# Kernel tuning notes

Measured on AMD Instinct MI355X. Metric: run time of the kernel, lower is better.

Reference implementation:

```python
import jax, jax.numpy as jnp
import numpy as np

B, A, D, H = 256, 16, 768, 512
LN_EPS = 1e-5


def setup_inputs() -> dict:
    key = jax.random.key(0)
    ks = jax.random.split(key, 8)
    aspects = jax.random.normal(ks[0], (B, A, D), dtype=jnp.float32)
    aspect_mask = jnp.ones((B, A), dtype=bool)
    # relation_gate: Linear(2D->H), ReLU, Dropout(eval=id), Linear(H->1)
    # xavier_uniform with gain=0.1, bias=-2.0 (per the module's custom init)
    lim1 = 0.1 * np.sqrt(6.0 / (2 * D + H))
    lim2 = 0.1 * np.sqrt(6.0 / (H + 1))
    W_g1 = jax.random.uniform(ks[1], (2 * D, H), jnp.float32, -lim1, lim1)
    b_g1 = jnp.full((H,), -2.0, dtype=jnp.float32)
    w_g2 = jax.random.uniform(ks[2], (H,), jnp.float32, -lim2, lim2)
    b_g2 = jnp.asarray(-2.0, dtype=jnp.float32)
    # composition: Linear(2D->H), ReLU, Dropout(eval=id), Linear(H->D), default init scale
    sc1 = 1.0 / np.sqrt(2 * D)
    sc2 = 1.0 / np.sqrt(H)
    W_c1 = jax.random.uniform(ks[3], (2 * D, H), jnp.float32, -sc1, sc1)
    b_c1 = jax.random.uniform(ks[4], (H,), jnp.float32, -sc1, sc1)
    W_c2 = jax.random.uniform(ks[5], (H, D), jnp.float32, -sc2, sc2)
    b_c2 = jax.random.uniform(ks[6], (D,), jnp.float32, -sc2, sc2)
    ln_gamma = jnp.ones((D,), dtype=jnp.float32)
    ln_beta = jnp.zeros((D,), dtype=jnp.float32)
    return {
        "aspects": aspects, "aspect_mask": aspect_mask,
        "W_g1": W_g1, "b_g1": b_g1, "w_g2": w_g2, "b_g2": b_g2,
        "W_c1": W_c1, "b_c1": b_c1, "W_c2": W_c2, "b_c2": b_c2,
        "ln_gamma": ln_gamma, "ln_beta": ln_beta,
    }


def reference(aspects, aspect_mask, W_g1, b_g1, w_g2, b_g2,
              W_c1, b_c1, W_c2, b_c2, ln_gamma, ln_beta):
    b, a, d = aspects.shape
    # cat([x_i, x_j]) @ W == x_i @ W[:D] + x_j @ W[D:]  -> batch all (i,j) pairs at once
    Wg_i, Wg_j = W_g1[:d], W_g1[d:]
    gi = jnp.einsum('bad,dh->bah', aspects, Wg_i)   # [B,A,H]
    gj = jnp.einsum('bad,dh->bah', aspects, Wg_j)   # [B,A,H]
    hg = jax.nn.relu(gi[:, :, None, :] + gj[:, None, :, :] + b_g1)  # [B,A,A,H]
    gate = jax.nn.sigmoid(jnp.einsum('bijh,h->bij', hg, w_g2) + b_g2)  # [B,A,A]
    eye = jnp.eye(a, dtype=bool)
    gate = jnp.where(eye[None], 0.0, gate)  # i==j pair skipped; all_gates diag stays 0

    Wc_i, Wc_j = W_c1[:d], W_c1[d:]
    ci = jnp.einsum('bad,dh->bah', aspects, Wc_i)
    cj = jnp.einsum('bad,dh->bah', aspects, Wc_j)
    hc = jax.nn.relu(ci[:, :, None, :] + cj[:, None, :, :] + b_c1)  # [B,A,A,H]
    composed = jnp.einsum('bijh,hd->bijd', hc, W_c2) + b_c2          # [B,A,A,D]
    # gated sum over source aspects j (gate is 0 on diag, masking i==j)
    influence = jnp.einsum('bij,bijd->bid', gate, composed)
    final = aspects + influence
    # LayerNorm over last dim
    mu = jnp.mean(final, axis=-1, keepdims=True)
    var = jnp.mean(jnp.square(final - mu), axis=-1, keepdims=True)
    final = (final - mu) * jax.lax.rsqrt(var + LN_EPS) * ln_gamma + ln_beta
    final = final * aspect_mask[..., None].astype(final.dtype)
    return final, gate
```

## Files before the change

### kernel.cpp

```cpp
#include <hip/hip_runtime.h>
#include <stdint.h>
#include <stddef.h>

typedef __attribute__((ext_vector_type(8))) short bf16x8;
typedef __attribute__((ext_vector_type(4))) float f32x4;
typedef __attribute__((ext_vector_type(8))) unsigned short u16x8;

typedef __attribute__((address_space(1))) unsigned int as1_u32;
typedef __attribute__((address_space(3))) unsigned int as3_u32;

__device__ __forceinline__ unsigned short f2b(float f) {
  union { unsigned int u; float f; } v; v.f = f;
  unsigned int u = v.u;
  return (unsigned short)((u + 0x7FFFu + ((u >> 16) & 1u)) >> 16);
}
__device__ __forceinline__ float b2f(unsigned short s) {
  union { unsigned int u; float f; } v; v.u = ((unsigned int)s) << 16; return v.f;
}
__device__ __forceinline__ void gld16(const unsigned short* g, unsigned short* l) {
  __builtin_amdgcn_global_load_lds((const as1_u32*)(unsigned int*)(size_t)(const void*)g,
                                   (as3_u32*)(unsigned int*)l, 16, 0, 0);
}

#define LN_EPS 1e-5f
#define BB 256
#define AA 16
#define DD 768
#define HH 512
#define ASTR 776

__global__ __launch_bounds__(256) void prep(const float* __restrict__ Wg1,
                                            const float* __restrict__ Wc1,
                                            const float* __restrict__ Wc2,
                                            const float* __restrict__ aspects,
                                            unsigned short* __restrict__ Wt,
                                            unsigned short* __restrict__ Wc2t,
                                            unsigned short* __restrict__ Abf) {
  const int seg = blockIdx.z;
  if (seg == 5) {
    const int id = (blockIdx.y * 24 + blockIdx.x) * 256 + threadIdx.x + threadIdx.y * 32;
    for (int g = id; g < 393216; g += 147456) {
      const size_t i = (size_t)g * 8;
      const float4 f0 = *(const float4*)(aspects + i);
      const float4 f1 = *(const float4*)(aspects + i + 4);
      u16x8 p;
      p[0] = f2b(f0.x); p[1] = f2b(f0.y); p[2] = f2b(f0.z); p[3] = f2b(f0.w);
      p[4] = f2b(f1.x); p[5] = f2b(f1.y); p[6] = f2b(f1.z); p[7] = f2b(f1.w);
      *(u16x8*)(Abf + i) = p;
    }
    return;
  }
  const float* src;
  unsigned short* dst;
  int R, C;
  if (seg < 4) {
    src = (seg < 2 ? Wg1 : Wc1) + (size_t)(seg & 1) * DD * HH;
    dst = Wt + (size_t)seg * HH * DD;
    R = DD; C = HH;
  } else {
    src = Wc2; dst = Wc2t; R = HH; C = DD;
  }
  const int c0 = blockIdx.x * 32, r0 = blockIdx.y * 32;
  if (c0 >= C || r0 >= R) return;
  __shared__ float t[32][33];
  const int x = threadIdx.x;
  for (int yy = threadIdx.y; yy < 32; yy += 8)
    t[yy][x] = src[(size_t)(r0 + yy) * C + (c0 + x)];
  __syncthreads();
  for (int yy = threadIdx.y; yy < 32; yy += 8)
    dst[(size_t)(c0 + yy) * R + (r0 + x)] = f2b(t[x][yy]);
}

__global__ __launch_bounds__(256) void gemm1(const unsigned short* __restrict__ A,
                                             const unsigned short* __restrict__ Bt,
                                             unsigned short* __restrict__ P) {
  const int bx = blockIdx.x;
  const int mb = bx & 31, nb = bx >> 5;
  const int tid = threadIdx.x;
  const int w = tid >> 6, lane = tid & 63;
  const int lr = lane & 15, quad = lane >> 4;
  const int m0 = (w & 1) * 64, n0 = (w >> 1) * 64;
  const int K = DD;

  __shared__ __align__(16) unsigned short As[128 * 64];
  __shared__ __align__(16) unsigned short Bs[128 * 64];

  f32x4 acc[4][4] = {};

  const unsigned short* gsrc[8];
  unsigned short* lbase[8];
#pragma unroll
  for (int i = 0; i < 8; ++i) {
    const int cb = w * 64 + i * 256;
    const int c = cb + lane;
    if (cb < 1024) {
      const int row = c >> 3, lcol = (c & 7) ^ (row & 7);
      gsrc[i]  = A + (size_t)(mb * 128 + row) * K + lcol * 8;
      lbase[i] = As + cb * 8;
    } else {
      const int p = c - 1024, row = p >> 3, lcol = (p & 7) ^ (row & 7);
      gsrc[i]  = Bt + (size_t)(nb * 128 + row) * K + lcol * 8;
      lbase[i] = Bs + (cb - 1024) * 8;
    }
  }

  for (int kk = 0; kk < K; kk += 64) {
    __syncthreads();
#pragma unroll
    for (int i = 0; i < 8; ++i) gld16(gsrc[i] + kk, lbase[i]);
    __syncthreads();
#pragma unroll
    for (int h = 0; h < 2; ++h) {
      bf16x8 a4[4], b4[4];
#pragma unroll
      for (int i = 0; i < 4; ++i) {
        const int row = m0 + i * 16 + lr;
        a4[i] = *(const bf16x8*)(As + row * 64 + (((quad + h * 4) ^ (row & 7)) * 8));
      }
#pragma unroll
      for (int j = 0; j < 4; ++j) {
        const int row = n0 + j * 16 + lr;
        b4[j] = *(const bf16x8*)(Bs + row * 64 + (((quad + h * 4) ^ (row & 7)) * 8));
      }
#pragma unroll
      for (int i = 0; i < 4; ++i)
#pragma unroll
        for (int j = 0; j < 4; ++j)
          acc[i][j] = __builtin_amdgcn_mfma_f32_16x16x32_bf16(a4[i], b4[j], acc[i][j], 0, 0, 0);
    }
  }

  const int rowb = mb * 128 + m0 + quad * 4;
  const int colb = nb * 128 + n0 + lr;
#pragma unroll
  for (int i = 0; i < 4; ++i)
#pragma unroll
    for (int j = 0; j < 4; ++j)
#pragma unroll
      for (int r = 0; r < 4; ++r)
        P[(size_t)(rowb + i * 16 + r) * 2048 + colb + j * 16] = f2b(acc[i][j][r]);
}

__global__ __launch_bounds__(512) void pairwise(const unsigned short* __restrict__ P,
                                                const float* __restrict__ bg1,
                                                const float* __restrict__ wg2,
                                                const float* __restrict__ bg2p,
                                                const float* __restrict__ bc1,
                                                unsigned short* __restrict__ u,
                                                float* __restrict__ gsum,
                                                float* __restrict__ gateO) {
  const int b = blockIdx.x;
  const int tid = threadIdx.x;
  const int v = tid >> 6;
  const int lane = tid & 63;
  __shared__ unsigned short S[16 * 2048];
  const unsigned short* Pb = P + (size_t)b * 16 * 2048;
#pragma unroll
  for (int i = 0; i < 8; ++i) {
    const int off = (tid + i * 512) * 8;
    *(u16x8*)(S + off) = *(const u16x8*)(Pb + off);
  }
  __syncthreads();

  float bg1v[8], wg2v[8], bc1v[8];
#pragma unroll
  for (int q = 0; q < 8; ++q) {
    const int h = lane + q * 64;
    bg1v[q] = bg1[h]; wg2v[q] = wg2[h]; bc1v[q] = bc1[h];
  }
  const float bg2s = bg2p[0];

  float giR[2][8], ciR[2][8];
#pragma unroll
  for (int r = 0; r < 2; ++r) {
    const int i = v * 2 + r;
#pragma unroll
    for (int q = 0; q < 8; ++q) {
      const int h = lane + q * 64;
      giR[r][q] = b2f(S[i * 2048 + h]);
      ciR[r][q] = b2f(S[i * 2048 + 1024 + h]);
    }
  }

  float uac[2][8] = {};
  float gs[2] = {0.f, 0.f};
  for (int j = 0; j < AA; ++j) {
    float gjq[8], cjq[8];
#pragma unroll
    for (int q = 0; q < 8; ++q) {
      const int h = lane + q * 64;
      gjq[q] = b2f(S[j * 2048 + 512 + h]);
      cjq[q] = b2f(S[j * 2048 + 1536 + h]);
    }
#pragma unroll
    for (int r = 0; r < 2; ++r) {
      const int i = v * 2 + r;
      float dot = 0.f;
#pragma unroll
      for (int q = 0; q < 8; ++q)
        dot = fmaf(fmaxf(giR[r][q] + gjq[q] + bg1v[q], 0.f), wg2v[q], dot);
#pragma unroll
      for (int off = 32; off; off >>= 1) dot += __shfl_xor(dot, off);
      float gate = (j == i) ? 0.f : (1.f / (1.f + __expf(-(dot + bg2s))));
      if (lane == 0) gateO[((size_t)b * 16 + i) * 16 + j] = gate;
      gs[r] += gate;
#pragma unroll
      for (int q = 0; q < 8; ++q)
        uac[r][q] = fmaf(gate, fmaxf(ciR[r][q] + cjq[q] + bc1v[q], 0.f), uac[r][q]);
    }
  }
#pragma unroll
  for (int r = 0; r < 2; ++r) {
    const int i = v * 2 + r;
#pragma unroll
    for (int q = 0; q < 8; ++q)
      u[(size_t)(b * 16 + i) * HH + lane + q * 64] = f2b(uac[r][q]);
    if (lane == 0) gsum[b * 16 + i] = gs[r];
  }
}

__global__ __launch_bounds__(512) void gemm2ln(const unsigned short* __restrict__ u,
                                               const unsigned short* __restrict__ Wc2t,
                                               const float* __restrict__ gsum,
                                               const float* __restrict__ aspects,
                                               const float* __restrict__ bc2,
                                               const float* __restrict__ gma,
                                               const float* __restrict__ bta,
                                               float* __restrict__ outF) {
  const int b = blockIdx.x;
  const int tid = threadIdx.x;
  const int v = tid >> 6;
  const int lane = tid & 63;
  const int lr = lane & 15, quad = lane >> 4;

  __shared__ float buf[4704];
  unsigned short* uS = (unsigned short*)buf;
  float* redS = buf + 4160;
  float* musS = buf + 4416;
  float* rsS  = buf + 4432;

  const unsigned short* ub = u + (size_t)b * 16 * HH;
#pragma unroll
  for (int it = 0; it < 2; ++it) {
    const int t = tid + it * 512;
    const int row = t >> 6, off = (t & 63) * 8;
    *(u16x8*)(uS + row * 520 + off) = *(const u16x8*)(ub + row * HH + off);
  }
  __syncthreads();

  f32x4 oc[6] = {};
  {
    const unsigned short* up = uS + lr * 520 + quad * 8;
    const unsigned short* wp = Wc2t + (size_t)(v * 96 + lr) * HH + quad * 8;
    bf16x8 c6[6], n6[6];
#pragma unroll
    for (int t = 0; t < 6; ++t) c6[t] = *(const bf16x8*)(wp + (size_t)t * (16 * HH));
    for (int kk = 0; kk < HH; kk += 64) {
#pragma unroll
      for (int t = 0; t < 6; ++t) n6[t] = *(const bf16x8*)(wp + (size_t)t * (16 * HH) + kk + 32);
      {
        bf16x8 af = *(const bf16x8*)(up + kk);
#pragma unroll
        for (int t = 0; t < 6; ++t)
          oc[t] = __builtin_amdgcn_mfma_f32_16x16x32_bf16(af, c6[t], oc[t], 0, 0, 0);
      }
      if (kk + 64 < HH) {
#pragma unroll
        for (int t = 0; t < 6; ++t) c6[t] = *(const bf16x8*)(wp + (size_t)t * (16 * HH) + kk + 64);
      }
      {
        bf16x8 af = *(const bf16x8*)(up + kk + 32);
#pragma unroll
        for (int t = 0; t < 6; ++t)
          oc[t] = __builtin_amdgcn_mfma_f32_16x16x32_bf16(af, n6[t], oc[t], 0, 0, 0);
      }
    }
  }

  float val[6][4];
  float s1p[4] = {0.f, 0.f, 0.f, 0.f}, s2p[4] = {0.f, 0.f, 0.f, 0.f};
  const int R0 = quad * 4;
  float gsv[4];
#pragma unroll
  for (int r = 0; r < 4; ++r) gsv[r] = gsum[(size_t)b * 16 + R0 + r];
#pragma unroll
  for (int t = 0; t < 6; ++t) {
    const int n = v * 96 + t * 16 + lr;
    const float bc2v = bc2[n];
#pragma unroll
    for (int r = 0; r < 4; ++r) {
      const size_t m = (size_t)b * 16 + R0 + r;
      const float x = oc[t][r] + gsv[r] * bc2v + aspects[m * DD + n];
      val[t][r] = x;
      s1p[r] += x;
      s2p[r] = fmaf(x, x, s2p[r]);
    }
  }
#pragma unroll
  for (int off = 8; off; off >>= 1)
#pragma unroll
    for (int r = 0; r < 4; ++r) {
      s1p[r] += __shfl_xor(s1p[r], off);
      s2p[r] += __shfl_xor(s2p[r], off);
    }
  if (lr == 0) {
#pragma unroll
    for (int r = 0; r < 4; ++r) {
      redS[(v * 16 + R0 + r) * 2 + 0] = s1p[r];
      redS[(v * 16 + R0 + r) * 2 + 1] = s2p[r];
    }
  }
  __syncthreads();
  if (tid < 16) {
    float s1 = 0.f, s2 = 0.f;
#pragma unroll
    for (int w = 0; w < 8; ++w) {
      s1 += redS[(w * 16 + tid) * 2 + 0];
      s2 += redS[(w * 16 + tid) * 2 + 1];
    }
    const float mu = s1 * (1.f / 768.f);
    const float var = s2 * (1.f / 768.f) - mu * mu;
    musS[tid] = mu;
    rsS[tid] = rsqrtf(var + LN_EPS);
  }
  __syncthreads();
#pragma unroll
  for (int t = 0; t < 6; ++t) {
    const int n = v * 96 + t * 16 + lr;
    const float g = gma[n], be = bta[n];
#pragma unroll
    for (int r = 0; r < 4; ++r) {
      const int row = R0 + r;
      outF[((size_t)b * 16 + row) * DD + n] = (val[t][r] - musS[row]) * rsS[row] * g + be;
    }
  }
}

extern "C" void kernel_launch(void* const* d_in, const int* in_sizes, int n_in,
                              void* d_out, int out_size, void* d_ws, size_t ws_size,
                              hipStream_t stream) {
  const float* aspects = (const float*)d_in[0];
  const float* W_g1 = (const float*)d_in[2];
  const float* b_g1 = (const float*)d_in[3];
  const float* w_g2 = (const float*)d_in[4];
  const float* b_g2 = (const float*)d_in[5];
  const float* W_c1 = (const float*)d_in[6];
  const float* b_c1 = (const float*)d_in[7];
  const float* W_c2 = (const float*)d_in[8];
  const float* b_c2 = (const float*)d_in[9];
  const float* ln_g = (const float*)d_in[10];
  const float* ln_b = (const float*)d_in[11];

  float* outF  = (float*)d_out;
  float* gateO = outF + (size_t)BB * AA * DD;

  char* ws = (char*)d_ws;
  unsigned short* Wt   = (unsigned short*)ws;
  unsigned short* Wc2t = (unsigned short*)(ws + 3145728);
  unsigned short* Abf  = (unsigned short*)(ws + 3932160);
  unsigned short* P    = (unsigned short*)(ws + 10223616);
  unsigned short* u    = (unsigned short*)(ws + 27000832);
  float* gsum          = (float*)(ws + 31195136);

  prep<<<dim3(24, 24, 6), dim3(32, 8, 1), 0, stream>>>(W_g1, W_c1, W_c2, aspects,
                                                       Wt, Wc2t, Abf);
  gemm1<<<512, 256, 0, stream>>>(Abf, Wt, P);
  pairwise<<<BB, 512, 0, stream>>>(P, b_g1, w_g2, b_g2, b_c1, u, gsum, gateO);
  gemm2ln<<<BB, 512, 0, stream>>>(u, Wc2t, gsum, aspects, b_c2, ln_g, ln_b, outF);
}
```

Before: 154.6 us.

## Fuse aspects bf16 conversion into gemm1 and double-buffer its K loop

Drops the separate fp32-to-bf16 conversion of the aspects tensor from the prep kernel. gemm1 now reads fp32 aspects directly, converts them in registers and writes swizzled bf16 tiles into shared memory. The K loop also gains double-buffered shared memory (64 KB), prefetching the next weight tile with global_load_lds and the next aspects tile into registers while the MFMAs run. This removes the Abf round-trip through global memory and halves the barriers per step, at the cost of more registers, more LDS per block and twice as much fp32 A-operand traffic per block.

After: 157.2 us. No clear change (+1.7%).

```diff
diff --git a/kernel.cpp b/kernel.cpp
--- a/kernel.cpp
+++ b/kernel.cpp
@@ -5,6 +5,7 @@
 typedef __attribute__((ext_vector_type(8))) short bf16x8;
 typedef __attribute__((ext_vector_type(4))) float f32x4;
 typedef __attribute__((ext_vector_type(8))) unsigned short u16x8;
+typedef __attribute__((ext_vector_type(4))) unsigned short u16x4;
 
 typedef __attribute__((address_space(1))) unsigned int as1_u32;
 typedef __attribute__((address_space(3))) unsigned int as3_u32;
@@ -27,29 +28,13 @@
 #define AA 16
 #define DD 768
 #define HH 512
-#define ASTR 776
 
 __global__ __launch_bounds__(256) void prep(const float* __restrict__ Wg1,
                                             const float* __restrict__ Wc1,
                                             const float* __restrict__ Wc2,
-                                            const float* __restrict__ aspects,
                                             unsigned short* __restrict__ Wt,
-                                            unsigned short* __restrict__ Wc2t,
-                                            unsigned short* __restrict__ Abf) {
+                                            unsigned short* __restrict__ Wc2t) {
   const int seg = blockIdx.z;
-  if (seg == 5) {
-    const int id = (blockIdx.y * 24 + blockIdx.x) * 256 + threadIdx.x + threadIdx.y * 32;
-    for (int g = id; g < 393216; g += 147456) {
-      const size_t i = (size_t)g * 8;
-      const float4 f0 = *(const float4*)(aspects + i);
-      const float4 f1 = *(const float4*)(aspects + i + 4);
-      u16x8 p;
-      p[0] = f2b(f0.x); p[1] = f2b(f0.y); p[2] = f2b(f0.z); p[3] = f2b(f0.w);
-      p[4] = f2b(f1.x); p[5] = f2b(f1.y); p[6] = f2b(f1.z); p[7] = f2b(f1.w);
-      *(u16x8*)(Abf + i) = p;
-    }
-    return;
-  }
   const float* src;
   unsigned short* dst;
   int R, C;
@@ -71,8 +56,8 @@
     dst[(size_t)(c0 + yy) * R + (r0 + x)] = f2b(t[x][yy]);
 }
 
-__global__ __launch_bounds__(256) void gemm1(const unsigned short* __restrict__ A,
-                                             const unsigned short* __restrict__ Bt,
+__global__ __launch_bounds__(256) void gemm1(const float* __restrict__ Asp,
+                                             const unsigned short* __restrict__ Wt,
                                              unsigned short* __restrict__ P) {
   const int bx = blockIdx.x;
   const int mb = bx & 31, nb = bx >> 5;
@@ -80,47 +65,65 @@
   const int w = tid >> 6, lane = tid & 63;
   const int lr = lane & 15, quad = lane >> 4;
   const int m0 = (w & 1) * 64, n0 = (w >> 1) * 64;
-  const int K = DD;
-
-  __shared__ __align__(16) unsigned short As[128 * 64];
-  __shared__ __align__(16) unsigned short Bs[128 * 64];
-
-  f32x4 acc[4][4] = {};
-
-  const unsigned short* gsrc[8];
-  unsigned short* lbase[8];
-#pragma unroll
-  for (int i = 0; i < 8; ++i) {
+
+  __shared__ __align__(16) unsigned short S[32768];
+
+  const unsigned short* bsrc[4];
+  int blofs[4];
+#pragma unroll
+  for (int i = 0; i < 4; ++i) {
     const int cb = w * 64 + i * 256;
     const int c = cb + lane;
-    if (cb < 1024) {
-      const int row = c >> 3, lcol = (c & 7) ^ (row & 7);
-      gsrc[i]  = A + (size_t)(mb * 128 + row) * K + lcol * 8;
-      lbase[i] = As + cb * 8;
-    } else {
-      const int p = c - 1024, row = p >> 3, lcol = (p & 7) ^ (row & 7);
-      gsrc[i]  = Bt + (size_t)(nb * 128 + row) * K + lcol * 8;
-      lbase[i] = Bs + (cb - 1024) * 8;
-    }
-  }
-
-  for (int kk = 0; kk < K; kk += 64) {
-    __syncthreads();
-#pragma unroll
-    for (int i = 0; i < 8; ++i) gld16(gsrc[i] + kk, lbase[i]);
-    __syncthreads();
+    const int row = c >> 3, lcol = (c & 7) ^ (row & 7);
+    bsrc[i]  = Wt + (size_t)(nb * 128 + row) * DD + lcol * 8;
+    blofs[i] = cb * 8;
+  }
+  const float* arow = Asp + (size_t)(mb * 128) * DD;
+
+  f32x4 acc[4][4] = {};
+
+#pragma unroll
+  for (int i = 0; i < 4; ++i) gld16(bsrc[i], S + 16384 + blofs[i]);
+#pragma unroll
+  for (int p = 0; p < 8; ++p) {
+    const int idx = p * 1024 + tid * 4;
+    const int m = idx >> 6, kl = idx & 63;
+    const float4 f = *(const float4*)(arow + (size_t)m * DD + kl);
+    u16x4 v; v[0] = f2b(f.x); v[1] = f2b(f.y); v[2] = f2b(f.z); v[3] = f2b(f.w);
+    *(u16x4*)(S + m * 64 + ((((kl >> 3) ^ (m & 7)) << 3) | (kl & 7))) = v;
+  }
+  __syncthreads();
+
+  for (int kk = 0; kk < 12; ++kk) {
+    const int par = kk & 1;
+    float4 af[8];
+    const bool more = (kk + 1 < 12);
+    if (more) {
+      const int np = par ^ 1;
+#pragma unroll
+      for (int i = 0; i < 4; ++i)
+        gld16(bsrc[i] + (kk + 1) * 64, S + 16384 + np * 8192 + blofs[i]);
+#pragma unroll
+      for (int p = 0; p < 8; ++p) {
+        const int idx = p * 1024 + tid * 4;
+        const int m = idx >> 6, kl = idx & 63;
+        af[p] = *(const float4*)(arow + (size_t)m * DD + (kk + 1) * 64 + kl);
+      }
+    }
+    const unsigned short* As = S + par * 8192;
+    const unsigned short* Bs = S + 16384 + par * 8192;
 #pragma unroll
     for (int h = 0; h < 2; ++h) {
       bf16x8 a4[4], b4[4];
 #pragma unroll
       for (int i = 0; i < 4; ++i) {
         const int row = m0 + i * 16 + lr;
-        a4[i] = *(const bf16x8*)(As + row * 64 + (((quad + h * 4) ^ (row & 7)) * 8));
+        a4[i] = *(const bf16x8*)(As + row * 64 + (((h * 4 + quad) ^ (row & 7)) << 3));
       }
 #pragma unroll
       for (int j = 0; j < 4; ++j) {
         const int row = n0 + j * 16 + lr;
-        b4[j] = *(const bf16x8*)(Bs + row * 64 + (((quad + h * 4) ^ (row & 7)) * 8));
+        b4[j] = *(const bf16x8*)(Bs + row * 64 + (((h * 4 + quad) ^ (row & 7)) << 3));
       }
 #pragma unroll
       for (int i = 0; i < 4; ++i)
@@ -128,6 +131,18 @@
         for (int j = 0; j < 4; ++j)
           acc[i][j] = __builtin_amdgcn_mfma_f32_16x16x32_bf16(a4[i], b4[j], acc[i][j], 0, 0, 0);
     }
+    if (more) {
+      unsigned short* An = S + (par ^ 1) * 8192;
+#pragma unroll
+      for (int p = 0; p < 8; ++p) {
+        const int idx = p * 1024 + tid * 4;
+        const int m = idx >> 6, kl = idx & 63;
+        u16x4 v;
+        v[0] = f2b(af[p].x); v[1] = f2b(af[p].y); v[2] = f2b(af[p].z); v[3] = f2b(af[p].w);
+        *(u16x4*)(An + m * 64 + ((((kl >> 3) ^ (m & 7)) << 3) | (kl & 7))) = v;
+      }
+    }
+    __syncthreads();
   }
 
   const int rowb = mb * 128 + m0 + quad * 4;
@@ -357,14 +372,12 @@
   char* ws = (char*)d_ws;
   unsigned short* Wt   = (unsigned short*)ws;
   unsigned short* Wc2t = (unsigned short*)(ws + 3145728);
-  unsigned short* Abf  = (unsigned short*)(ws + 3932160);
-  unsigned short* P    = (unsigned short*)(ws + 10223616);
-  unsigned short* u    = (unsigned short*)(ws + 27000832);
-  float* gsum          = (float*)(ws + 31195136);
-
-  prep<<<dim3(24, 24, 6), dim3(32, 8, 1), 0, stream>>>(W_g1, W_c1, W_c2, aspects,
-                                                       Wt, Wc2t, Abf);
-  gemm1<<<512, 256, 0, stream>>>(Abf, Wt, P);
+  unsigned short* P    = (unsigned short*)(ws + 3932160);
+  unsigned short* u    = (unsigned short*)(ws + 20709376);
+  float* gsum          = (float*)(ws + 24903680);
+
+  prep<<<dim3(24, 24, 5), dim3(32, 8, 1), 0, stream>>>(W_g1, W_c1, W_c2, Wt, Wc2t);
+  gemm1<<<512, 256, 0, stream>>>(aspects, Wt, P);
   pairwise<<<BB, 512, 0, stream>>>(P, b_g1, w_g2, b_g2, b_c1, u, gsum, gateO);
   gemm2ln<<<BB, 512, 0, stream>>>(u, Wc2t, gsum, aspects, b_c2, ln_g, ln_b, outF);
 }
```
